# Kernel tuning notes

Hardware: AMD Instinct MI355X
Metric: run time of the kernel (lower is better)

## Reference

```python
import jax, jax.numpy as jnp
import numpy as np

NUM_CLASSES = 20
NUM_ANCHORS = 5
INPUT_SIZE = 320.0
CONF_THR = 0.5
IOU_THR = 0.5
EPS = 1e-6
H = W = 40


def setup_inputs() -> dict:
    key = jax.random.key(0)
    x = jax.random.normal(key, (1, NUM_ANCHORS * (5 + NUM_CLASSES), H, W), dtype=jnp.float32)
    scaled_anchors = jnp.array(
        [[1.3221, 1.73145], [3.19275, 4.00944], [5.05587, 8.09892],
         [9.47112, 4.84053], [11.2364, 10.0071]], dtype=jnp.float32)
    return {"x": x, "scaled_anchors": scaled_anchors}


def decode(x, anchors):
    # x: (B, A*(5+C), H, W) -> boxes (B, A*H*W, 6) = [cx, cy, w, h, conf, cls]
    B, _, h, w = x.shape
    A = anchors.shape[0]
    stride_h = INPUT_SIZE / h
    stride_w = INPUT_SIZE / w
    pred = x.reshape(B, A, 5 + NUM_CLASSES, h, w).transpose(0, 1, 3, 4, 2)  # (B,A,H,W,5+C)
    tx = jax.nn.sigmoid(pred[..., 0])
    ty = jax.nn.sigmoid(pred[..., 1])
    tw = pred[..., 2]
    th = pred[..., 3]
    conf = jax.nn.sigmoid(pred[..., 4])
    cls_idx = jnp.argmax(jax.nn.sigmoid(pred[..., 5:]), axis=-1)  # (B,A,H,W)
    grid_x = jnp.arange(w, dtype=x.dtype)            # broadcasts along last axis
    grid_y = jnp.arange(h, dtype=x.dtype)[:, None]   # broadcasts along row axis
    aw = anchors[:, 0][None, :, None, None]
    ah = anchors[:, 1][None, :, None, None]
    bx = (tx + grid_x) * stride_w
    by = (ty + grid_y) * stride_h
    bw = jnp.exp(tw) * aw * stride_w
    bh = jnp.exp(th) * ah * stride_h
    boxes = jnp.stack([bx, by, bw, bh, conf], axis=-1).reshape(B, -1, 5)
    cls_f = cls_idx.reshape(B, -1, 1).astype(x.dtype)
    return jnp.concatenate([boxes, cls_f], axis=-1)


def nms(boxes6):
    # boxes6: (N, 6) [cx, cy, w, h, conf, cls]. Fixed-shape NMS: boxes are
    # sorted by conf desc; suppressed / low-conf boxes are zeroed out.
    order = jnp.argsort(-boxes6[:, 4])
    b = boxes6[order]
    valid = b[:, 4] > CONF_THR
    cx, cy, w, h, cls = b[:, 0], b[:, 1], b[:, 2], b[:, 3], b[:, 5]
    x1, y1 = cx - w / 2.0, cy - h / 2.0
    x2, y2 = cx + w / 2.0, cy + h / 2.0
    inter_w = jnp.clip(jnp.minimum(x2[:, None], x2[None, :]) - jnp.maximum(x1[:, None], x1[None, :]), 0)
    inter_h = jnp.clip(jnp.minimum(y2[:, None], y2[None, :]) - jnp.maximum(y1[:, None], y1[None, :]), 0)
    inter = inter_w * inter_h                       # (N, N)
    area = jnp.abs((x2 - x1) * (y2 - y1))
    iou = inter / (area[:, None] + area[None, :] - inter + EPS)
    N = b.shape[0]
    idx = jnp.arange(N)

    def body(i, keep):
        # kept box i suppresses later boxes of the same class with IoU >= thr
        sup = keep[i] & keep & (cls == cls[i]) & (iou[i] >= IOU_THR) & (idx > i)
        return keep & ~sup

    keep = jax.lax.fori_loop(0, N, body, valid)
    return b * keep[:, None].astype(b.dtype)


def reference(x, scaled_anchors):
    dec = decode(x, scaled_anchors)   # (1, N, 6)
    return nms(dec[0])                # (N, 6)
```

## Files before the change

kernel.cpp:

```cpp
#include <hip/hip_runtime.h>
#include <stdint.h>

#define NBOX 8000
#define NPAD 8192

#define ECNT_OFF 0
#define SB(i)    (0x10000 + (size_t)(i) * 0x8000)
#define EDGE_OFF (size_t)0x200000

__device__ __forceinline__ float sigmoidf_(float x) {
    return 1.0f / (1.0f + expf(-x));
}

__global__ __launch_bounds__(256) void sort_decode_kernel(const float* __restrict__ x,
                                                          const float* __restrict__ anchors,
                                                          unsigned char* __restrict__ ws) {
    __shared__ unsigned long long tile[256];
    __shared__ int partial[256];
    int tid  = threadIdx.x;
    int lane = tid & 63;
    int q    = tid >> 6;
    int b    = blockIdx.x;
    int i    = (b << 6) + lane;

    if (b == 0 && tid == 0) *(unsigned int*)(ws + ECNT_OFF) = 0u;

    unsigned long long ki;
    if (i < NBOX) {
        int a = i / 1600, pos = i - a * 1600;
        float c = sigmoidf_(x[a * 40000 + 4 * 1600 + pos]);
        ki = ((unsigned long long)__float_as_uint(c) << 32) | (unsigned long long)(8191 - i);
    } else {
        ki = (unsigned long long)(8191 - i);
    }

    int cnt = 0;
    for (int tb = 0; tb < 32; ++tb) {
        int j = (tb << 8) + tid;
        unsigned long long kj;
        if (j < NBOX) {
            int aj = j / 1600, posj = j - aj * 1600;
            float cj = sigmoidf_(x[aj * 40000 + 4 * 1600 + posj]);
            kj = ((unsigned long long)__float_as_uint(cj) << 32) | (unsigned long long)(8191 - j);
        } else {
            kj = (unsigned long long)(8191 - j);
        }
        tile[tid] = kj;
        __syncthreads();
        const unsigned long long* tq = &tile[q << 6];
        #pragma unroll 16
        for (int jj = 0; jj < 64; ++jj) cnt += (tq[jj] > ki) ? 1 : 0;
        __syncthreads();
    }
    partial[tid] = cnt;
    __syncthreads();

    if (q == 0) {
        int r = partial[lane] + partial[64 + lane] + partial[128 + lane] + partial[192 + lane];
        float bx = 0.f, by = 0.f, bw = 0.f, bh = 0.f, conf = 0.f, cls = -1.0f;
        if (i < NBOX) {
            int a = i / 1600, pos = i - a * 1600;
            int gy = pos / 40, gx = pos - gy * 40;
            const float* p = x + (size_t)a * 40000 + pos;
            float tx = sigmoidf_(p[0]);
            float ty = sigmoidf_(p[1600]);
            float tw = p[2 * 1600];
            float th = p[3 * 1600];
            conf = sigmoidf_(p[4 * 1600]);
            float best = -1.0f; int bi = 0;
            #pragma unroll
            for (int c = 0; c < 20; ++c) {
                float v = sigmoidf_(p[(5 + c) * 1600]);
                if (v > best) { best = v; bi = c; }
            }
            float aw = anchors[a * 2 + 0];
            float ah = anchors[a * 2 + 1];
            bx = (tx + (float)gx) * 8.0f;
            by = (ty + (float)gy) * 8.0f;
            bw = expf(tw) * aw * 8.0f;
            bh = expf(th) * ah * 8.0f;
            cls = (float)bi;
        }
        {
        #pragma clang fp contract(off)
            float x1 = bx - bw / 2.0f, y1 = by - bh / 2.0f;
            float x2 = bx + bw / 2.0f, y2 = by + bh / 2.0f;
            float ar = fabsf((x2 - x1) * (y2 - y1));
            ((float*)(ws + SB(0)))[r]  = bx;  ((float*)(ws + SB(1)))[r]  = by;
            ((float*)(ws + SB(2)))[r]  = bw;  ((float*)(ws + SB(3)))[r]  = bh;
            ((float*)(ws + SB(4)))[r]  = conf; ((float*)(ws + SB(5)))[r] = cls;
            ((float*)(ws + SB(6)))[r]  = x1;  ((float*)(ws + SB(7)))[r]  = y1;
            ((float*)(ws + SB(8)))[r]  = x2;  ((float*)(ws + SB(9)))[r]  = y2;
            ((float*)(ws + SB(10)))[r] = ar;
        }
    }
}

__global__ __launch_bounds__(256) void mask_kernel(unsigned char* __restrict__ ws) {
#pragma clang fp contract(off)
    const float* sconf = (const float*)(ws + SB(4));
    int i0 = blockIdx.y * 256;
    int w  = blockIdx.x;
    int j0 = w * 64;
    if (sconf[i0] <= 0.5f) return;
    if (sconf[j0] <= 0.5f) return;
    if (j0 + 64 <= i0) return;
    int tid  = threadIdx.x;
    int lane = tid & 63;
    int i    = i0 + tid;

    const float* sx1 = (const float*)(ws + SB(6));
    const float* sy1 = (const float*)(ws + SB(7));
    const float* sx2 = (const float*)(ws + SB(8));
    const float* sy2 = (const float*)(ws + SB(9));
    const float* sar = (const float*)(ws + SB(10));
    const float* scl = (const float*)(ws + SB(5));

    __shared__ float cx1[64], cy1[64], cx2[64], cy2[64], car[64], ccl[64], ccf[64];
    if (tid < 64) {
        int j = j0 + tid;
        cx1[tid] = sx1[j]; cy1[tid] = sy1[j];
        cx2[tid] = sx2[j]; cy2[tid] = sy2[j];
        car[tid] = sar[j]; ccl[tid] = scl[j]; ccf[tid] = sconf[j];
    }
    __syncthreads();

    unsigned long long word = 0;
    if (sconf[i] > 0.5f && j0 + 64 > i + 1) {
        float x1i = sx1[i], y1i = sy1[i], x2i = sx2[i], y2i = sy2[i];
        float ai = sar[i], ci = scl[i];
        for (int jj = 0; jj < 64; ++jj) {
            int j = j0 + jj;
            if (j <= i) continue;
            if (ccf[jj] <= 0.5f) continue;
            if (ccl[jj] != ci) continue;
            float iw = fminf(x2i, cx2[jj]) - fmaxf(x1i, cx1[jj]);
            iw = fmaxf(iw, 0.0f);
            float ih = fminf(y2i, cy2[jj]) - fmaxf(y1i, cy1[jj]);
            ih = fmaxf(ih, 0.0f);
            float inter = iw * ih;
            float denom = ai + car[jj] - inter + 1e-6f;
            if (inter / denom >= 0.5f) word |= (1ull << jj);
        }
    }

    int pc = __popcll(word);
    int scan = pc;
    #pragma unroll
    for (int d = 1; d < 64; d <<= 1) {
        int t = __shfl_up(scan, d, 64);
        if (lane >= d) scan += t;
    }
    int total = __shfl(scan, 63, 64);
    if (total > 0) {
        unsigned int base = 0;
        if (lane == 63)
            base = atomicAdd((unsigned int*)(ws + ECNT_OFF), (unsigned int)total);
        base = (unsigned int)__shfl((int)base, 63, 64);
        unsigned int off = base + (unsigned int)(scan - pc);
        unsigned int* edges = (unsigned int*)(ws + EDGE_OFF);
        unsigned long long t = word;
        while (t) {
            int bit = __builtin_ctzll(t);
            t &= t - 1ull;
            edges[off++] = ((unsigned int)i << 13) | (unsigned int)(j0 + bit);
        }
    }
}

__global__ __launch_bounds__(1024, 1) void nms_out_kernel(unsigned char* __restrict__ ws,
                                                          float* __restrict__ out) {
    int tid  = threadIdx.x;
    int lane = tid & 63;
    unsigned int E = *(const unsigned int*)(ws + ECNT_OFF);
    const unsigned int* edges = (const unsigned int*)(ws + EDGE_OFF);
    const float* sconf = (const float*)(ws + SB(4));

    __shared__ unsigned long long valid[128], alive[128], supp[128];
    __shared__ int flag;

    for (int c = tid >> 6; c < 128; c += 16) {
        unsigned long long m = __ballot(sconf[(c << 6) + lane] > 0.5f);
        if (lane == 0) valid[c] = m;
    }
    __syncthreads();
    if (tid < 128) alive[tid] = valid[tid];
    __syncthreads();

    for (;;) {
        if (tid < 128) supp[tid] = 0ull;
        __syncthreads();
        for (unsigned int e = tid; e < E; e += 1024) {
            unsigned int u = edges[e];
            unsigned int i = u >> 13, j = u & 8191u;
            if ((alive[i >> 6] >> (i & 63)) & 1ull)
                atomicOr(&supp[j >> 6], 1ull << (j & 63));
        }
        if (tid == 0) flag = 0;
        __syncthreads();
        if (tid < 128) {
            unsigned long long na = valid[tid] & ~supp[tid];
            if (na != alive[tid]) { alive[tid] = na; flag = 1; }
        }
        __syncthreads();
        if (!flag) break;
    }

    for (int r = tid; r < NBOX; r += 1024) {
        bool keep = (alive[r >> 6] >> (r & 63)) & 1ull;
        float o0 = 0.f, o1 = 0.f, o2 = 0.f, o3 = 0.f, o4 = 0.f, o5 = 0.f;
        if (keep) {
            o0 = ((const float*)(ws + SB(0)))[r];
            o1 = ((const float*)(ws + SB(1)))[r];
            o2 = ((const float*)(ws + SB(2)))[r];
            o3 = ((const float*)(ws + SB(3)))[r];
            o4 = ((const float*)(ws + SB(4)))[r];
            o5 = ((const float*)(ws + SB(5)))[r];
        }
        out[r * 6 + 0] = o0;
        out[r * 6 + 1] = o1;
        out[r * 6 + 2] = o2;
        out[r * 6 + 3] = o3;
        out[r * 6 + 4] = o4;
        out[r * 6 + 5] = o5;
    }
}

extern "C" void kernel_launch(void* const* d_in, const int* in_sizes, int n_in,
                              void* d_out, int out_size, void* d_ws, size_t ws_size,
                              hipStream_t stream) {
    const float* x       = (const float*)d_in[0];
    const float* anchors = (const float*)d_in[1];
    float* out           = (float*)d_out;
    unsigned char* ws    = (unsigned char*)d_ws;

    sort_decode_kernel<<<NPAD / 64, 256, 0, stream>>>(x, anchors, ws);
    dim3 mgrid(128, NPAD / 256);
    mask_kernel<<<mgrid, 256, 0, stream>>>(ws);
    nms_out_kernel<<<1, 1024, 0, stream>>>(ws, out);
}
```

Measured before the change: 136.7 us.

## Stage all sort keys in LDS once and rank against 1024-key chunks per wave

The rank-sort kernel now has each 512-thread block compute all 8192 confidence keys into a 64 KB shared array with one barrier. Each of its 8 waves then counts against a contiguous 1024-key slice, instead of streaming 32 tiles through shared memory with two barriers per tile. This removes many block-level synchronisations and repeated small tile loads. In exchange, each block recomputes every key, and the large LDS footprint limits how many blocks fit per CU.

```diff
diff --git a/kernel.cpp b/kernel.cpp
--- a/kernel.cpp
+++ b/kernel.cpp
@@ -12,51 +12,45 @@
     return 1.0f / (1.0f + expf(-x));
 }
 
-__global__ __launch_bounds__(256) void sort_decode_kernel(const float* __restrict__ x,
+__global__ __launch_bounds__(512) void sort_decode_kernel(const float* __restrict__ x,
                                                           const float* __restrict__ anchors,
                                                           unsigned char* __restrict__ ws) {
-    __shared__ unsigned long long tile[256];
-    __shared__ int partial[256];
+    __shared__ unsigned long long keys[NPAD];
+    __shared__ int partial[512];
     int tid  = threadIdx.x;
     int lane = tid & 63;
-    int q    = tid >> 6;
+    int wv   = tid >> 6;
     int b    = blockIdx.x;
-    int i    = (b << 6) + lane;
 
     if (b == 0 && tid == 0) *(unsigned int*)(ws + ECNT_OFF) = 0u;
 
-    unsigned long long ki;
-    if (i < NBOX) {
-        int a = i / 1600, pos = i - a * 1600;
-        float c = sigmoidf_(x[a * 40000 + 4 * 1600 + pos]);
-        ki = ((unsigned long long)__float_as_uint(c) << 32) | (unsigned long long)(8191 - i);
-    } else {
-        ki = (unsigned long long)(8191 - i);
-    }
-
+    for (int t = tid; t < NPAD; t += 512) {
+        unsigned long long k;
+        if (t < NBOX) {
+            int a = t / 1600, pos = t - a * 1600;
+            float c = sigmoidf_(x[a * 40000 + 4 * 1600 + pos]);
+            k = ((unsigned long long)__float_as_uint(c) << 32) | (unsigned long long)(8191 - t);
+        } else {
+            k = (unsigned long long)(8191 - t);
+        }
+        keys[t] = k;
+    }
+    __syncthreads();
+
+    int i = (b << 6) + lane;
+    unsigned long long ki = keys[i];
+    const unsigned long long* ks = &keys[wv << 10];
     int cnt = 0;
-    for (int tb = 0; tb < 32; ++tb) {
-        int j = (tb << 8) + tid;
-        unsigned long long kj;
-        if (j < NBOX) {
-            int aj = j / 1600, posj = j - aj * 1600;
-            float cj = sigmoidf_(x[aj * 40000 + 4 * 1600 + posj]);
-            kj = ((unsigned long long)__float_as_uint(cj) << 32) | (unsigned long long)(8191 - j);
-        } else {
-            kj = (unsigned long long)(8191 - j);
-        }
-        tile[tid] = kj;
-        __syncthreads();
-        const unsigned long long* tq = &tile[q << 6];
-        #pragma unroll 16
-        for (int jj = 0; jj < 64; ++jj) cnt += (tq[jj] > ki) ? 1 : 0;
-        __syncthreads();
-    }
-    partial[tid] = cnt;
-    __syncthreads();
-
-    if (q == 0) {
-        int r = partial[lane] + partial[64 + lane] + partial[128 + lane] + partial[192 + lane];
+    #pragma unroll 8
+    for (int jj = 0; jj < 1024; ++jj) cnt += (ks[jj] > ki) ? 1 : 0;
+    partial[(wv << 6) + lane] = cnt;
+    __syncthreads();
+
+    if (wv == 0) {
+        int r = 0;
+        #pragma unroll
+        for (int s = 0; s < 8; ++s) r += partial[(s << 6) + lane];
+
         float bx = 0.f, by = 0.f, bw = 0.f, bh = 0.f, conf = 0.f, cls = -1.0f;
         if (i < NBOX) {
             int a = i / 1600, pos = i - a * 1600;
@@ -234,7 +228,7 @@
     float* out           = (float*)d_out;
     unsigned char* ws    = (unsigned char*)d_ws;
 
-    sort_decode_kernel<<<NPAD / 64, 256, 0, stream>>>(x, anchors, ws);
+    sort_decode_kernel<<<NPAD / 64, 512, 0, stream>>>(x, anchors, ws);
     dim3 mgrid(128, NPAD / 256);
     mask_kernel<<<mgrid, 256, 0, stream>>>(ws);
     nms_out_kernel<<<1, 1024, 0, stream>>>(ws, out);
```

Measured after the change: 120.2 us. 1.14x faster.
